# Kernel optimization log

Measured on AMD Instinct MI355X. Metric: run time of the kernel, lower is better.

The kernel has to match this reference:

```python
import jax, jax.numpy as jnp
import numpy as np

D_MODEL = 1024
N_HEADS = 16
HEAD_DIM = D_MODEL // N_HEADS


def setup_inputs() -> dict:
    key = jax.random.key(0)
    ks = jax.random.split(key, 9)
    B, T, S, D = 4, 2048, 512, D_MODEL
    sc = 1.0 / np.sqrt(D)
    return {
        "x": jax.random.normal(ks[0], (B, T, D), dtype=jnp.float32),
        "context": jax.random.normal(ks[1], (B, S, D), dtype=jnp.float32),
        "context_mask": jnp.ones((B, S), dtype=bool),
        "Wq": jax.random.normal(ks[2], (D, D), dtype=jnp.float32) * sc,
        "bq": jnp.zeros((D,), dtype=jnp.float32),
        "Wkv": jax.random.normal(ks[3], (D, 2 * D), dtype=jnp.float32) * sc,
        "bkv": jnp.zeros((2 * D,), dtype=jnp.float32),
        "Wp": jax.random.normal(ks[4], (D, D), dtype=jnp.float32) * sc,
        "bp": jnp.zeros((D,), dtype=jnp.float32),
    }


def reference(x, context, context_mask, Wq, bq, Wkv, bkv, Wp, bp):
    B, T, D = x.shape
    S = context.shape[1]
    H, Hd = N_HEADS, HEAD_DIM
    # projections
    q = (x @ Wq + bq).reshape(B, T, H, Hd).transpose(0, 2, 1, 3)          # [B,H,T,Hd]
    kv = (context @ Wkv + bkv).reshape(B, S, 2, H, Hd)
    k = kv[:, :, 0].transpose(0, 2, 1, 3)                                  # [B,H,S,Hd]
    v = kv[:, :, 1].transpose(0, 2, 1, 3)                                  # [B,H,S,Hd]
    # scaled dot-product attention with context mask
    scores = jnp.einsum("bhtd,bhsd->bhts", q, k) / np.sqrt(Hd)            # [B,H,T,S]
    neg_inf = jnp.finfo(scores.dtype).min
    scores = jnp.where(context_mask[:, None, None, :], scores, neg_inf)
    attn = jax.nn.softmax(scores, axis=-1)
    # dropout is identity in eval mode (p applied only in training)
    out = jnp.einsum("bhts,bhsd->bthd", attn, v).reshape(B, T, D)
    return out @ Wp + bp
```

## Files before the change

### kernel.cpp

```cpp
#include <hip/hip_runtime.h>

typedef __bf16 bf16x8 __attribute__((ext_vector_type(8)));
typedef float  f32x4  __attribute__((ext_vector_type(4)));

#define MFMA(a, b, c) __builtin_amdgcn_mfma_f32_16x16x32_bf16((a), (b), (c), 0, 0, 0)

#define GLL(g, l) __builtin_amdgcn_global_load_lds(                                  \
    (const __attribute__((address_space(1))) void*)(g),                              \
    (__attribute__((address_space(3))) void*)(l), 16, 0, 0)

#define BB 4
#define TT 2048
#define SS 512
#define DM 1024
#define NH 16
#define HD 64

__device__ __forceinline__ unsigned short f2b(float f) {
    union { float f; unsigned int u; } v; v.f = f;
    unsigned int r = (v.u + 0x7fffu + ((v.u >> 16) & 1u)) >> 16;
    return (unsigned short)r;
}

__device__ __forceinline__ void tcast_tile(const float* __restrict__ in,
                                           unsigned short* __restrict__ out,
                                           int K, int N, int n0, int k0,
                                           float (*tile)[33], int tid) {
    int tx = tid & 31, ty = tid >> 5;
#pragma unroll
    for (int r = 0; r < 32; r += 8)
        tile[ty + r][tx] = in[(k0 + ty + r) * N + n0 + tx];
    __syncthreads();
#pragma unroll
    for (int r = 0; r < 32; r += 8)
        out[(n0 + ty + r) * K + k0 + tx] = f2b(tile[tx][ty + r]);
}

__global__ __launch_bounds__(256)
void prep(const float4* __restrict__ x, const float4* __restrict__ ctx,
          const unsigned int* __restrict__ mw,
          const float* __restrict__ Wq, const float* __restrict__ Wkv,
          const float* __restrict__ Wp,
          ushort4* __restrict__ Xbf, ushort4* __restrict__ Cbf,
          unsigned short* __restrict__ WqT, unsigned short* __restrict__ WkvT,
          unsigned short* __restrict__ WpT, float* __restrict__ mbias) {
    __shared__ float tile[32][33];
    __shared__ int flags[2];
    const int bid = blockIdx.x, tid = threadIdx.x;
    if (bid < 8192) {
        int i = bid * 256 + tid;
        float4 v = x[i];
        ushort4 o; o.x = f2b(v.x); o.y = f2b(v.y); o.z = f2b(v.z); o.w = f2b(v.w);
        Xbf[i] = o;
    } else if (bid < 10240) {
        int i = (bid - 8192) * 256 + tid;
        float4 v = ctx[i];
        ushort4 o; o.x = f2b(v.x); o.y = f2b(v.y); o.z = f2b(v.z); o.w = f2b(v.w);
        Cbf[i] = o;
    } else if (bid < 11264) {
        int loc = bid - 10240;
        tcast_tile(Wq, WqT, DM, DM, (loc & 31) * 32, (loc >> 5) * 32, tile, tid);
    } else if (bid < 13312) {
        int loc = bid - 11264;
        tcast_tile(Wkv, WkvT, DM, 2 * DM, (loc & 63) * 32, (loc >> 6) * 32, tile, tid);
    } else if (bid < 14336) {
        int loc = bid - 13312;
        tcast_tile(Wp, WpT, DM, DM, (loc & 31) * 32, (loc >> 5) * 32, tile, tid);
    } else {
        if (tid == 0) { flags[0] = 1; flags[1] = 1; }
        __syncthreads();
        int okI = 1, okF = 1;
        for (int i = tid; i < 512; i += 256) {
            unsigned int w = mw[i];
            if (w > 1u) okI = 0;
            if (w != 0u && w != 0x3f800000u) okF = 0;
        }
        if (!okI) atomicAnd(&flags[0], 0);
        if (!okF) atomicAnd(&flags[1], 0);
        __syncthreads();
        bool wordLayout = (flags[0] != 0) || (flags[1] != 0);
        const unsigned char* mb = (const unsigned char*)mw;
        for (int s = tid; s < BB * SS; s += 256) {
            bool on = wordLayout ? (mw[s] != 0u) : (mb[s] != 0);
            mbias[s] = on ? 0.0f : -1e38f;
        }
    }
}

template <int MODE>
__global__ __launch_bounds__(128, 4)
void gemm_w2(const unsigned short* __restrict__ A, const unsigned short* __restrict__ Bt,
             const float* __restrict__ bias, unsigned short* __restrict__ out_u16,
             float* __restrict__ out_f32, int M, int N, int K) {
    __shared__ __align__(16) unsigned short As[128 * 32];
    __shared__ __align__(16) unsigned short Bs[64 * 32];
    const int tid = threadIdx.x;
    const int w = tid >> 6, l = tid & 63;
    const int quad = l >> 4, col = l & 15;
    const int m0 = blockIdx.x * 128, n0 = blockIdx.y * 64;
    const int wm = w * 64;

    const int r = tid >> 2, c = (tid & 3) * 8;
    const unsigned short* Ab = A + (m0 + r) * K + c;
    const unsigned short* Bb = Bt + (n0 + r) * K + c;

    const f32x4 zero = {0.f, 0.f, 0.f, 0.f};
    f32x4 acc[4][4];
#pragma unroll
    for (int i = 0; i < 4; i++)
#pragma unroll
        for (int j = 0; j < 4; j++) acc[i][j] = zero;

    for (int k0 = 0; k0 < K; k0 += 32) {
        __syncthreads();
        GLL(Ab + k0,            &As[tid * 8]);
        GLL(Ab + k0 + 32 * K,   &As[(tid + 128) * 8]);
        GLL(Ab + k0 + 64 * K,   &As[(tid + 256) * 8]);
        GLL(Ab + k0 + 96 * K,   &As[(tid + 384) * 8]);
        GLL(Bb + k0,            &Bs[tid * 8]);
        GLL(Bb + k0 + 32 * K,   &Bs[(tid + 128) * 8]);
        __syncthreads();
        bf16x8 af[4], bf[4];
#pragma unroll
        for (int i = 0; i < 4; i++) af[i] = *(const bf16x8*)&As[(wm + i * 16 + col) * 32 + quad * 8];
#pragma unroll
        for (int j = 0; j < 4; j++) bf[j] = *(const bf16x8*)&Bs[(j * 16 + col) * 32 + quad * 8];
#pragma unroll
        for (int i = 0; i < 4; i++)
#pragma unroll
            for (int j = 0; j < 4; j++) acc[i][j] = MFMA(af[i], bf[j], acc[i][j]);
    }

#pragma unroll
    for (int i = 0; i < 4; i++) {
#pragma unroll
        for (int j = 0; j < 4; j++) {
            int n = n0 + j * 16 + col;
            int mb = m0 + wm + i * 16 + quad * 4;
            float bv = bias[n];
            f32x4 cc = acc[i][j];
            if (MODE == 0) {
                const float QS = 0.125f * 1.4426950408889634f;
#pragma unroll
                for (int ii = 0; ii < 4; ii++)
                    out_u16[(mb + ii) * N + n] = f2b((cc[ii] + bv) * QS);
            } else {
#pragma unroll
                for (int ii = 0; ii < 4; ii++)
                    out_f32[(mb + ii) * N + n] = cc[ii] + bv;
            }
        }
    }
}

__global__ __launch_bounds__(256, 4)
void gemm_kv(const unsigned short* __restrict__ A, const unsigned short* __restrict__ Bt,
             const float* __restrict__ bias, unsigned short* __restrict__ out_k,
             unsigned short* __restrict__ out_v, int M, int N, int K) {
    __shared__ __align__(16) unsigned short As[128 * 32];
    __shared__ __align__(16) unsigned short Bs[64 * 32];
    const int tid = threadIdx.x;
    const int w = tid >> 6, l = tid & 63;
    const int quad = l >> 4, col = l & 15;
    const int m0 = blockIdx.x * 128, n0 = blockIdx.y * 64;
    const int wm = w * 32;

    const int idx = tid * 8;
    const int r = tid >> 2, c = (tid & 3) * 8;

    const f32x4 zero = {0.f, 0.f, 0.f, 0.f};
    f32x4 acc[2][4];
#pragma unroll
    for (int i = 0; i < 2; i++)
#pragma unroll
        for (int j = 0; j < 4; j++) acc[i][j] = zero;

    for (int k0 = 0; k0 < K; k0 += 32) {
        __syncthreads();
        GLL(&A[(m0 + r) * K + k0 + c], &As[idx]);
        GLL(&A[(m0 + 64 + r) * K + k0 + c], &As[idx + 2048]);
        GLL(&Bt[(n0 + r) * K + k0 + c], &Bs[idx]);
        __syncthreads();
        bf16x8 af[2], bfr[4];
#pragma unroll
        for (int i = 0; i < 2; i++) af[i]  = *(const bf16x8*)&As[(wm + i * 16 + col) * 32 + quad * 8];
#pragma unroll
        for (int j = 0; j < 4; j++) bfr[j] = *(const bf16x8*)&Bs[(j * 16 + col) * 32 + quad * 8];
#pragma unroll
        for (int i = 0; i < 2; i++)
#pragma unroll
            for (int j = 0; j < 4; j++) acc[i][j] = MFMA(af[i], bfr[j], acc[i][j]);
    }

#pragma unroll
    for (int i = 0; i < 2; i++) {
#pragma unroll
        for (int j = 0; j < 4; j++) {
            int n = n0 + j * 16 + col;
            int mb = m0 + wm + i * 16 + quad * 4;
            float bv = bias[n];
            f32x4 cc = acc[i][j];
            if (n < 1024) {
                int h = n >> 6, d = n & 63;
#pragma unroll
                for (int ii = 0; ii < 4; ii++) {
                    int m = mb + ii; int b = m >> 9, s = m & 511;
                    out_k[(((b * NH + h) * SS) + s) * HD + d] = f2b(cc[ii] + bv);
                }
            } else {
                int q = n - 1024; int h = q >> 6, d = q & 63;
#pragma unroll
                for (int ii = 0; ii < 4; ii++) {
                    int m = mb + ii; int b = m >> 9, s = m & 511;
                    out_v[(((b * NH + h) * HD) + d) * SS + s] = f2b(cc[ii] + bv);
                }
            }
        }
    }
}

__global__ __launch_bounds__(512, 4)
void flash_attn(const unsigned short* __restrict__ Q, const unsigned short* __restrict__ Kb,
                const unsigned short* __restrict__ Vt, const float* __restrict__ mbias,
                unsigned short* __restrict__ O) {
    const int bid = blockIdx.x;
    const int tb = bid & 7, bh = bid >> 3;
    const int b = bh >> 4;
    const int tid = threadIdx.x;
    const int w = tid >> 6, l = tid & 63;
    const int quad = l >> 4, col = l & 15;

    __shared__ __align__(16) unsigned short Ks[2][64 * 64];
    __shared__ __align__(16) unsigned short Vs[2][64 * 64];
    __shared__ __align__(16) unsigned short Pb[8][32 * 40];
    __shared__ float biasS[SS];

    const unsigned short* Kh = Kb + bh * SS * HD;
    const unsigned short* Vh = Vt + bh * HD * SS;

    biasS[tid] = mbias[b * SS + tid];

    const int rowbase = b * TT + tb * 256 + w * 32;
    bf16x8 qf[2][2];
#pragma unroll
    for (int rg = 0; rg < 2; rg++) {
        const unsigned short* qrow = Q + (rowbase + rg * 16 + col) * DM + (bh & 15) * HD;
        qf[rg][0] = *(const bf16x8*)(qrow + quad * 8);
        qf[rg][1] = *(const bf16x8*)(qrow + 32 + quad * 8);
    }

    const int sr = tid >> 3, sp = tid & 7;
    const int spk = ((sp ^ (sr & 7)) * 8);
    const int kgo = sr * HD + spk;
    const int vgo = sr * SS + spk;

    GLL(Kh + kgo, &Ks[0][tid * 8]);
    GLL(Vh + vgo, &Vs[0][tid * 8]);

    const f32x4 zero = {0.f, 0.f, 0.f, 0.f};
    f32x4 o[2][4];
#pragma unroll
    for (int rg = 0; rg < 2; rg++)
#pragma unroll
        for (int j = 0; j < 4; j++) o[rg][j] = zero;
    f32x4 lsum[2] = {zero, zero};

    for (int it = 0; it < SS / 64; ++it) {
        const int s0 = it * 64;
        const int buf = it & 1;
        __syncthreads();
        if (it + 1 < SS / 64) {
            GLL(Kh + (s0 + 64) * HD + kgo, &Ks[buf ^ 1][tid * 8]);
            GLL(Vh + (s0 + 64) + vgo, &Vs[buf ^ 1][tid * 8]);
        }

#pragma unroll
        for (int h2 = 0; h2 < 2; ++h2) {
            f32x4 sc[2][2];
#pragma unroll
            for (int jj = 0; jj < 2; ++jj) {
                int row = (2 * h2 + jj) * 16 + col;
                bf16x8 k0 = *(const bf16x8*)&Ks[buf][row * 64 + ((quad ^ (row & 7)) * 8)];
                bf16x8 k1 = *(const bf16x8*)&Ks[buf][row * 64 + (((4 + quad) ^ (row & 7)) * 8)];
#pragma unroll
                for (int rg = 0; rg < 2; rg++) {
                    f32x4 t = MFMA(qf[rg][0], k0, zero);
                    sc[rg][jj] = MFMA(qf[rg][1], k1, t);
                }
            }
#pragma unroll
            for (int rg = 0; rg < 2; rg++) {
#pragma unroll
                for (int jj = 0; jj < 2; jj++) {
                    float bb = biasS[s0 + (2 * h2 + jj) * 16 + col];
#pragma unroll
                    for (int i = 0; i < 4; i++) {
                        float p = exp2f(sc[rg][jj][i] + bb);
                        lsum[rg][i] += p;
                        Pb[w][(rg * 16 + quad * 4 + i) * 40 + jj * 16 + col] = f2b(p);
                    }
                }
            }
            asm volatile("s_waitcnt lgkmcnt(0)" ::: "memory");
            bf16x8 pf[2];
#pragma unroll
            for (int rg = 0; rg < 2; rg++)
                pf[rg] = *(const bf16x8*)&Pb[w][(rg * 16 + col) * 40 + quad * 8];
#pragma unroll
            for (int j2 = 0; j2 < 4; j2++) {
                int row = j2 * 16 + col;
                bf16x8 vf = *(const bf16x8*)&Vs[buf][row * 64 + (((h2 * 4 + quad) ^ (row & 7)) * 8)];
#pragma unroll
                for (int rg = 0; rg < 2; rg++)
                    o[rg][j2] = MFMA(pf[rg], vf, o[rg][j2]);
            }
            asm volatile("" ::: "memory");
        }
    }

#pragma unroll
    for (int rg = 0; rg < 2; rg++) {
#pragma unroll
        for (int i = 0; i < 4; i++) {
            float rs = lsum[rg][i];
#pragma unroll
            for (int off = 1; off < 16; off <<= 1) rs += __shfl_xor(rs, off);
            float inv = 1.0f / rs;
            unsigned short* orow = O + (rowbase + rg * 16 + quad * 4 + i) * DM
                                     + (bh & 15) * HD + col;
#pragma unroll
            for (int j2 = 0; j2 < 4; j2++)
                orow[j2 * 16] = f2b(o[rg][j2][i] * inv);
        }
    }
}

extern "C" void kernel_launch(void* const* d_in, const int* in_sizes, int n_in,
                              void* d_out, int out_size, void* d_ws, size_t ws_size,
                              hipStream_t stream) {
    const float* x    = (const float*)d_in[0];
    const float* ctx  = (const float*)d_in[1];
    const void*  cmsk = d_in[2];
    const float* Wq   = (const float*)d_in[3];
    const float* bq   = (const float*)d_in[4];
    const float* Wkv  = (const float*)d_in[5];
    const float* bkv  = (const float*)d_in[6];
    const float* Wp   = (const float*)d_in[7];
    const float* bp   = (const float*)d_in[8];
    float* out = (float*)d_out;

    char* ws = (char*)d_ws;
    size_t off = 0;
    auto alloc = [&](size_t bytes) -> void* {
        void* p = ws + off;
        off += (bytes + 255) & ~(size_t)255;
        return p;
    };
    const size_t NX = (size_t)BB * TT * DM;
    const size_t NC = (size_t)BB * SS * DM;
    unsigned short* Xbf  = (unsigned short*)alloc(NX * 2);
    unsigned short* Cbf  = (unsigned short*)alloc(NC * 2);
    unsigned short* WqT  = (unsigned short*)alloc((size_t)DM * DM * 2);
    unsigned short* WkvT = (unsigned short*)alloc((size_t)DM * 2 * DM * 2);
    unsigned short* WpT  = (unsigned short*)alloc((size_t)DM * DM * 2);
    unsigned short* Qb   = (unsigned short*)alloc(NX * 2);
    unsigned short* Kbf  = (unsigned short*)alloc(NC * 2);
    unsigned short* Vtb  = (unsigned short*)alloc(NC * 2);
    unsigned short* Ob   = (unsigned short*)alloc(NX * 2);
    float* mbias         = (float*)alloc((size_t)BB * SS * 4);

    prep<<<14337, 256, 0, stream>>>((const float4*)x, (const float4*)ctx,
                                    (const unsigned int*)cmsk, Wq, Wkv, Wp,
                                    (ushort4*)Xbf, (ushort4*)Cbf,
                                    WqT, WkvT, WpT, mbias);

    gemm_w2<0><<<dim3(64, 16), 128, 0, stream>>>(Xbf, WqT, bq, Qb, nullptr,
                                                 BB * TT, DM, DM);
    gemm_kv<<<dim3(16, 32), 256, 0, stream>>>(Cbf, WkvT, bkv, Kbf, Vtb,
                                              BB * SS, 2 * DM, DM);
    flash_attn<<<BB * NH * (TT / 256), 512, 0, stream>>>(Qb, Kbf, Vtb, mbias, Ob);
    gemm_w2<2><<<dim3(64, 16), 128, 0, stream>>>(Ob, WpT, bp, nullptr, out,
                                                 BB * TT, DM, DM);
}
```

Baseline: 225.8 us.

## Merge Q and KV projections into one launch with swizzled K=64 GEMM tiles

Replaces the separate Q and KV projection GEMMs with a single grid whose blocks branch on their index. This removes one launch and lets the two GEMMs share the device. A shared gemm_core loads 64-wide K slices per barrier pair instead of 32 and XOR-swizzles the LDS layout to avoid bank conflicts. The KV path now uses 128-thread blocks with 4x4 accumulators. Manual bf16 rounding is swapped for the compiler's native bf16 cast. The larger LDS tiles and lower occupancy hint (3) may reduce how many blocks fit per CU.

```diff
diff --git a/kernel.cpp b/kernel.cpp
--- a/kernel.cpp
+++ b/kernel.cpp
@@ -20,6 +20,11 @@
     union { float f; unsigned int u; } v; v.f = f;
     unsigned int r = (v.u + 0x7fffu + ((v.u >> 16) & 1u)) >> 16;
     return (unsigned short)r;
+}
+__device__ __forceinline__ unsigned short f2bh(float f) {
+    __bf16 h = (__bf16)f;
+    union { __bf16 h; unsigned short u; } v; v.h = h;
+    return v.u;
 }
 
 __device__ __forceinline__ void tcast_tile(const float* __restrict__ in,
@@ -87,134 +92,146 @@
     }
 }
 
-template <int MODE>
-__global__ __launch_bounds__(128, 4)
-void gemm_w2(const unsigned short* __restrict__ A, const unsigned short* __restrict__ Bt,
-             const float* __restrict__ bias, unsigned short* __restrict__ out_u16,
-             float* __restrict__ out_f32, int M, int N, int K) {
-    __shared__ __align__(16) unsigned short As[128 * 32];
-    __shared__ __align__(16) unsigned short Bs[64 * 32];
+__device__ __forceinline__ void gemm_core(
+    const unsigned short* __restrict__ A, const unsigned short* __restrict__ Bt,
+    int K, int m0, int n0, unsigned short* As, unsigned short* Bs,
+    f32x4 (*acc)[4]) {
     const int tid = threadIdx.x;
     const int w = tid >> 6, l = tid & 63;
     const int quad = l >> 4, col = l & 15;
-    const int m0 = blockIdx.x * 128, n0 = blockIdx.y * 64;
     const int wm = w * 64;
-
-    const int r = tid >> 2, c = (tid & 3) * 8;
-    const unsigned short* Ab = A + (m0 + r) * K + c;
-    const unsigned short* Bb = Bt + (n0 + r) * K + c;
-
-    const f32x4 zero = {0.f, 0.f, 0.f, 0.f};
-    f32x4 acc[4][4];
-#pragma unroll
-    for (int i = 0; i < 4; i++)
-#pragma unroll
-        for (int j = 0; j < 4; j++) acc[i][j] = zero;
-
-    for (int k0 = 0; k0 < K; k0 += 32) {
-        __syncthreads();
-        GLL(Ab + k0,            &As[tid * 8]);
-        GLL(Ab + k0 + 32 * K,   &As[(tid + 128) * 8]);
-        GLL(Ab + k0 + 64 * K,   &As[(tid + 256) * 8]);
-        GLL(Ab + k0 + 96 * K,   &As[(tid + 384) * 8]);
-        GLL(Bb + k0,            &Bs[tid * 8]);
-        GLL(Bb + k0 + 32 * K,   &Bs[(tid + 128) * 8]);
-        __syncthreads();
-        bf16x8 af[4], bf[4];
-#pragma unroll
-        for (int i = 0; i < 4; i++) af[i] = *(const bf16x8*)&As[(wm + i * 16 + col) * 32 + quad * 8];
-#pragma unroll
-        for (int j = 0; j < 4; j++) bf[j] = *(const bf16x8*)&Bs[(j * 16 + col) * 32 + quad * 8];
-#pragma unroll
-        for (int i = 0; i < 4; i++)
-#pragma unroll
-            for (int j = 0; j < 4; j++) acc[i][j] = MFMA(af[i], bf[j], acc[i][j]);
-    }
-
-#pragma unroll
-    for (int i = 0; i < 4; i++) {
-#pragma unroll
-        for (int j = 0; j < 4; j++) {
-            int n = n0 + j * 16 + col;
-            int mb = m0 + wm + i * 16 + quad * 4;
-            float bv = bias[n];
-            f32x4 cc = acc[i][j];
-            if (MODE == 0) {
-                const float QS = 0.125f * 1.4426950408889634f;
-#pragma unroll
-                for (int ii = 0; ii < 4; ii++)
-                    out_u16[(mb + ii) * N + n] = f2b((cc[ii] + bv) * QS);
-            } else {
-#pragma unroll
-                for (int ii = 0; ii < 4; ii++)
-                    out_f32[(mb + ii) * N + n] = cc[ii] + bv;
-            }
-        }
-    }
-}
-
-__global__ __launch_bounds__(256, 4)
-void gemm_kv(const unsigned short* __restrict__ A, const unsigned short* __restrict__ Bt,
-             const float* __restrict__ bias, unsigned short* __restrict__ out_k,
-             unsigned short* __restrict__ out_v, int M, int N, int K) {
-    __shared__ __align__(16) unsigned short As[128 * 32];
-    __shared__ __align__(16) unsigned short Bs[64 * 32];
+    const int arow = tid >> 3;
+    const int apiece = (tid & 7) ^ (arow & 7);
+    const unsigned short* Ab = A + (size_t)(m0 + arow) * K + apiece * 8;
+    const unsigned short* Bb = Bt + (size_t)(n0 + arow) * K + apiece * 8;
+
+    for (int k0 = 0; k0 < K; k0 += 64) {
+        __syncthreads();
+#pragma unroll
+        for (int g = 0; g < 8; ++g)
+            GLL(Ab + k0 + g * 16 * K, &As[g * 1024 + tid * 8]);
+#pragma unroll
+        for (int g = 0; g < 4; ++g)
+            GLL(Bb + k0 + g * 16 * K, &Bs[g * 1024 + tid * 8]);
+        __syncthreads();
+#pragma unroll
+        for (int k32 = 0; k32 < 2; ++k32) {
+            bf16x8 af[4], bf[4];
+#pragma unroll
+            for (int i = 0; i < 4; i++) {
+                int rr = wm + i * 16 + col;
+                af[i] = *(const bf16x8*)&As[rr * 64 + (((k32 * 4 + quad) ^ (rr & 7)) * 8)];
+            }
+#pragma unroll
+            for (int j = 0; j < 4; j++) {
+                int rr = j * 16 + col;
+                bf[j] = *(const bf16x8*)&Bs[rr * 64 + (((k32 * 4 + quad) ^ (rr & 7)) * 8)];
+            }
+#pragma unroll
+            for (int i = 0; i < 4; i++)
+#pragma unroll
+                for (int j = 0; j < 4; j++) acc[i][j] = MFMA(af[i], bf[j], acc[i][j]);
+        }
+    }
+}
+
+__global__ __launch_bounds__(128, 3)
+void gemm_qkv(const unsigned short* __restrict__ Xbf, const unsigned short* __restrict__ WqT,
+              const float* __restrict__ bq, unsigned short* __restrict__ Qb,
+              const unsigned short* __restrict__ Cbf, const unsigned short* __restrict__ WkvT,
+              const float* __restrict__ bkv, unsigned short* __restrict__ Kb,
+              unsigned short* __restrict__ Vtb) {
+    __shared__ __align__(16) unsigned short As[128 * 64];
+    __shared__ __align__(16) unsigned short Bs[64 * 64];
     const int tid = threadIdx.x;
     const int w = tid >> 6, l = tid & 63;
     const int quad = l >> 4, col = l & 15;
-    const int m0 = blockIdx.x * 128, n0 = blockIdx.y * 64;
-    const int wm = w * 32;
-
-    const int idx = tid * 8;
-    const int r = tid >> 2, c = (tid & 3) * 8;
+    const int bid = blockIdx.x;
 
     const f32x4 zero = {0.f, 0.f, 0.f, 0.f};
-    f32x4 acc[2][4];
-#pragma unroll
-    for (int i = 0; i < 2; i++)
+    f32x4 acc[4][4];
+#pragma unroll
+    for (int i = 0; i < 4; i++)
 #pragma unroll
         for (int j = 0; j < 4; j++) acc[i][j] = zero;
 
-    for (int k0 = 0; k0 < K; k0 += 32) {
-        __syncthreads();
-        GLL(&A[(m0 + r) * K + k0 + c], &As[idx]);
-        GLL(&A[(m0 + 64 + r) * K + k0 + c], &As[idx + 2048]);
-        GLL(&Bt[(n0 + r) * K + k0 + c], &Bs[idx]);
-        __syncthreads();
-        bf16x8 af[2], bfr[4];
-#pragma unroll
-        for (int i = 0; i < 2; i++) af[i]  = *(const bf16x8*)&As[(wm + i * 16 + col) * 32 + quad * 8];
-#pragma unroll
-        for (int j = 0; j < 4; j++) bfr[j] = *(const bf16x8*)&Bs[(j * 16 + col) * 32 + quad * 8];
-#pragma unroll
-        for (int i = 0; i < 2; i++)
-#pragma unroll
-            for (int j = 0; j < 4; j++) acc[i][j] = MFMA(af[i], bfr[j], acc[i][j]);
-    }
-
-#pragma unroll
-    for (int i = 0; i < 2; i++) {
+    if (bid < 1024) {
+        const int m0 = (bid >> 4) * 128, n0 = (bid & 15) * 64;
+        gemm_core(Xbf, WqT, DM, m0, n0, As, Bs, acc);
+        const float QS = 0.125f * 1.4426950408889634f;
+#pragma unroll
+        for (int i = 0; i < 4; i++) {
+#pragma unroll
+            for (int j = 0; j < 4; j++) {
+                int n = n0 + j * 16 + col;
+                int mb = m0 + w * 64 + i * 16 + quad * 4;
+                float bv = bq[n];
+#pragma unroll
+                for (int ii = 0; ii < 4; ii++)
+                    Qb[(mb + ii) * DM + n] = f2bh((acc[i][j][ii] + bv) * QS);
+            }
+        }
+    } else {
+        const int loc = bid - 1024;
+        const int m0 = (loc >> 5) * 128, n0 = (loc & 31) * 64;
+        gemm_core(Cbf, WkvT, DM, m0, n0, As, Bs, acc);
+#pragma unroll
+        for (int i = 0; i < 4; i++) {
+#pragma unroll
+            for (int j = 0; j < 4; j++) {
+                int n = n0 + j * 16 + col;
+                int mb = m0 + w * 64 + i * 16 + quad * 4;
+                float bv = bkv[n];
+                if (n < 1024) {
+                    int h = n >> 6, d = n & 63;
+#pragma unroll
+                    for (int ii = 0; ii < 4; ii++) {
+                        int m = mb + ii; int b = m >> 9, s = m & 511;
+                        Kb[(((b * NH + h) * SS) + s) * HD + d] = f2bh(acc[i][j][ii] + bv);
+                    }
+                } else {
+                    int q = n - 1024; int h = q >> 6, d = q & 63;
+#pragma unroll
+                    for (int ii = 0; ii < 4; ii++) {
+                        int m = mb + ii; int b = m >> 9, s = m & 511;
+                        Vtb[(((b * NH + h) * HD) + d) * SS + s] = f2bh(acc[i][j][ii] + bv);
+                    }
+                }
+            }
+        }
+    }
+}
+
+__global__ __launch_bounds__(128, 3)
+void gemm_out(const unsigned short* __restrict__ Ob, const unsigned short* __restrict__ WpT,
+              const float* __restrict__ bp, float* __restrict__ out) {
+    __shared__ __align__(16) unsigned short As[128 * 64];
+    __shared__ __align__(16) unsigned short Bs[64 * 64];
+    const int tid = threadIdx.x;
+    const int w = tid >> 6, l = tid & 63;
+    const int quad = l >> 4, col = l & 15;
+    const int bid = blockIdx.x;
+    const int m0 = (bid >> 4) * 128, n0 = (bid & 15) * 64;
+
+    const f32x4 zero = {0.f, 0.f, 0.f, 0.f};
+    f32x4 acc[4][4];
+#pragma unroll
+    for (int i = 0; i < 4; i++)
+#pragma unroll
+        for (int j = 0; j < 4; j++) acc[i][j] = zero;
+
+    gemm_core(Ob, WpT, DM, m0, n0, As, Bs, acc);
+
+#pragma unroll
+    for (int i = 0; i < 4; i++) {
 #pragma unroll
         for (int j = 0; j < 4; j++) {
             int n = n0 + j * 16 + col;
-            int mb = m0 + wm + i * 16 + quad * 4;
-            float bv = bias[n];
-            f32x4 cc = acc[i][j];
-            if (n < 1024) {
-                int h = n >> 6, d = n & 63;
-#pragma unroll
-                for (int ii = 0; ii < 4; ii++) {
-                    int m = mb + ii; int b = m >> 9, s = m & 511;
-                    out_k[(((b * NH + h) * SS) + s) * HD + d] = f2b(cc[ii] + bv);
-                }
-            } else {
-                int q = n - 1024; int h = q >> 6, d = q & 63;
-#pragma unroll
-                for (int ii = 0; ii < 4; ii++) {
-                    int m = mb + ii; int b = m >> 9, s = m & 511;
-                    out_v[(((b * NH + h) * HD) + d) * SS + s] = f2b(cc[ii] + bv);
-                }
-            }
+            int mb = m0 + w * 64 + i * 16 + quad * 4;
+            float bv = bp[n];
+#pragma unroll
+            for (int ii = 0; ii < 4; ii++)
+                out[(mb + ii) * DM + n] = acc[i][j][ii] + bv;
         }
     }
 }
@@ -297,7 +314,7 @@
                     for (int i = 0; i < 4; i++) {
                         float p = exp2f(sc[rg][jj][i] + bb);
                         lsum[rg][i] += p;
-                        Pb[w][(rg * 16 + quad * 4 + i) * 40 + jj * 16 + col] = f2b(p);
+                        Pb[w][(rg * 16 + quad * 4 + i) * 40 + jj * 16 + col] = f2bh(p);
                     }
                 }
             }
@@ -330,7 +347,7 @@
                                      + (bh & 15) * HD + col;
 #pragma unroll
             for (int j2 = 0; j2 < 4; j2++)
-                orow[j2 * 16] = f2b(o[rg][j2][i] * inv);
+                orow[j2 * 16] = f2bh(o[rg][j2][i] * inv);
         }
     }
 }
@@ -374,11 +391,9 @@
                                     (ushort4*)Xbf, (ushort4*)Cbf,
                                     WqT, WkvT, WpT, mbias);
 
-    gemm_w2<0><<<dim3(64, 16), 128, 0, stream>>>(Xbf, WqT, bq, Qb, nullptr,
-                                                 BB * TT, DM, DM);
-    gemm_kv<<<dim3(16, 32), 256, 0, stream>>>(Cbf, WkvT, bkv, Kbf, Vtb,
-                                              BB * SS, 2 * DM, DM);
+    gemm_qkv<<<1536, 128, 0, stream>>>(Xbf, WqT, bq, Qb, Cbf, WkvT, bkv, Kbf, Vtb);
+
     flash_attn<<<BB * NH * (TT / 256), 512, 0, stream>>>(Qb, Kbf, Vtb, mbias, Ob);
-    gemm_w2<2><<<dim3(64, 16), 128, 0, stream>>>(Ob, WpT, bp, nullptr, out,
-                                                 BB * TT, DM, DM);
-}
+
+    gemm_out<<<1024, 128, 0, stream>>>(Ob, WpT, bp, out);
+}
```

Result: faster. 214.2 us (-5.1%).
